# Kernel tuning notes

Hardware: AMD Instinct MI355X
Metric: run time of the kernel (lower is better)

The kernel has to match this reference:

```python
import jax, jax.numpy as jnp
import numpy as np

N = 131072          # total instances
G = 2048            # n_groups
MAX = 128           # padded max group size (>= true max by construction)
E = 256             # embed_dim
H = 8               # num_heads
D = E // H          # head dim


def setup_inputs() -> dict:
    key = jax.random.key(0)
    ks = jax.random.split(key, 9)
    # every group id appears at least once (matches torch.unique-derived groups)
    gids = jnp.concatenate([
        jnp.arange(G, dtype=jnp.int32),
        jax.random.randint(ks[0], (N - G,), 0, G, dtype=jnp.int32),
    ])
    return {
        "tree_preds": jax.random.normal(ks[1], (N, E), dtype=jnp.float32),
        "group_ids": gids,
        "query": jax.random.normal(ks[2], (1, 1, E), dtype=jnp.float32) * 0.02,
        "w_in": jax.random.normal(ks[3], (3 * E, E), dtype=jnp.float32) * 0.02,
        "b_in": jax.random.normal(ks[4], (3 * E,), dtype=jnp.float32) * 0.02,
        "w_out": jax.random.normal(ks[5], (E, E), dtype=jnp.float32) * 0.02,
        "b_out": jax.random.normal(ks[6], (E,), dtype=jnp.float32) * 0.02,
        "w_lin": jax.random.normal(ks[7], (1, E), dtype=jnp.float32) * 0.02,
        "b_lin": jax.random.normal(ks[8], (1,), dtype=jnp.float32) * 0.02,
    }


def _forward(tree_preds, group_ids, query, w_in, b_in, w_out, b_out, w_lin, b_lin):
    # --- scatter ragged groups into padded [G, MAX, E] tensor ---
    sorter = jnp.argsort(group_ids)                   # stable instance sorter
    sorted_gid = group_ids[sorter]
    sizes = jax.ops.segment_sum(jnp.ones_like(group_ids), group_ids,
                                num_segments=G)       # [G] group sizes
    offsets = jnp.cumsum(sizes) - sizes               # exclusive cumsum
    pos = jnp.arange(N, dtype=sizes.dtype) - offsets[sorted_gid]  # slot in group
    embs = jnp.zeros((G, MAX, E), dtype=tree_preds.dtype)
    embs = embs.at[sorted_gid, pos].set(tree_preds[sorter])
    kp_mask = jnp.arange(MAX)[None, :] >= sizes[:, None]          # [G, MAX] True=pad

    # --- single-query multi-head attention pooling ---
    wq, wk, wv = w_in[:E], w_in[E:2 * E], w_in[2 * E:]
    bq, bk, bv = b_in[:E], b_in[E:2 * E], b_in[2 * E:]
    q = (query.reshape(E) @ wq.T + bq).reshape(H, D)              # shared query
    k = (embs @ wk.T + bk).reshape(G, MAX, H, D)
    v = (embs @ wv.T + bv).reshape(G, MAX, H, D)
    scores = jnp.einsum("hd,gmhd->ghm", q, k) / jnp.sqrt(jnp.float32(D))
    scores = jnp.where(kp_mask[:, None, :], -jnp.inf, scores)
    attn = jax.nn.softmax(scores, axis=-1)                        # [G, H, MAX]
    pooled = jnp.einsum("ghm,gmhd->ghd", attn, v).reshape(G, E)
    pooled = pooled @ w_out.T + b_out                             # out_proj
    return pooled @ w_lin.T + b_lin                               # [G, 1]


def reference(tree_preds, group_ids, query, w_in, b_in, w_out, b_out, w_lin, b_lin):
    return _forward(tree_preds, group_ids, query, w_in, b_in,
                    w_out, b_out, w_lin, b_lin)
```

## Files before the change

### kernel.cpp

```cpp
#include <hip/hip_runtime.h>
#include <hip/hip_bf16.h>

#define EDIM 256
#define INV_SQRT_D 0.17677669529663688f
#define FXSCALE 1099511627776.0f

#define WS_QB   4096
#define WS_UB   4104
#define WS_C    4112
#define WS_QS   4128
#define WS_PU   4608
#define WB_BYTE_OFF 36864
#define ZM_BYTE_OFF 65536

typedef __attribute__((ext_vector_type(8))) short short8;
typedef __attribute__((ext_vector_type(4))) float f32x4;

__device__ __forceinline__ unsigned short f2bf(float f) {
  unsigned u = __float_as_uint(f);
  unsigned r = (u + 0x7fffu + ((u >> 16) & 1u)) >> 16;
  return (unsigned short)r;
}

__global__ __launch_bounds__(256) void zero_zm(unsigned long long* __restrict__ zm, int n) {
  const int i = blockIdx.x * 256 + threadIdx.x;
  const int stride = gridDim.x * 256;
  for (int k = i; k < n; k += stride) zm[k] = 0ull;
}

__global__ __launch_bounds__(256) void prep1(
    const float* __restrict__ query, const float* __restrict__ w_in,
    const float* __restrict__ b_in, const float* __restrict__ w_out,
    const float* __restrict__ w_lin, float* __restrict__ ws) {
  const int b = blockIdx.x, t = threadIdx.x;
  if (b < 32) {
    const int r = b * 8 + (t >> 5);
    const int l = t & 31;
    const float4 q0 = *(const float4*)(query + l * 8);
    const float4 q1 = *(const float4*)(query + l * 8 + 4);
    const float4 w0 = *(const float4*)(w_in + (size_t)r * EDIM + l * 8);
    const float4 w1 = *(const float4*)(w_in + (size_t)r * EDIM + l * 8 + 4);
    float a = q0.x * w0.x + q0.y * w0.y + q0.z * w0.z + q0.w * w0.w
            + q1.x * w1.x + q1.y * w1.y + q1.z * w1.z + q1.w * w1.w;
    for (int m = 16; m >= 1; m >>= 1) a += __shfl_xor(a, m, 32);
    if (l == 0) ws[WS_QS + r] = a + b_in[r];
  } else {
    const int k = b - 32;
    float acc = 0.f;
#pragma unroll
    for (int f = 0; f < 16; ++f) {
      const int fr = k * 16 + f;
      acc += w_lin[fr] * w_out[(size_t)fr * EDIM + t];
    }
    ws[WS_PU + k * EDIM + t] = acc;
  }
}

__global__ __launch_bounds__(256) void prep2(
    const float* __restrict__ w_in, const float* __restrict__ b_in,
    const float* __restrict__ b_out, const float* __restrict__ b_lin,
    const float* __restrict__ w_lin, float* __restrict__ ws,
    unsigned short* __restrict__ wb) {
  const int b = blockIdx.x, t = threadIdx.x;
  if (b < 8) {
    __shared__ float qh[32];
    if (t < 32) qh[t] = ws[WS_QS + b * 32 + t];
    __syncthreads();
    float a = 0.f;
#pragma unroll 8
    for (int d = 0; d < 32; ++d)
      a += qh[d] * w_in[(size_t)(EDIM + b * 32 + d) * EDIM + t];
    wb[b * EDIM + t] = f2bf(a * INV_SQRT_D);
  } else if (b < 16) {
    const int j = b - 8;
    __shared__ float uh[32];
    if (t < 32) {
      float s = 0.f;
#pragma unroll
      for (int k = 0; k < 16; ++k) s += ws[WS_PU + k * EDIM + j * 32 + t];
      uh[t] = s;
    }
    __syncthreads();
    float a = 0.f;
#pragma unroll 8
    for (int d = 0; d < 32; ++d)
      a += uh[d] * w_in[(size_t)(2 * EDIM + j * 32 + d) * EDIM + t];
    wb[(8 + j) * EDIM + t] = f2bf(a);
  } else {
    __shared__ float us[EDIM];
    float s = 0.f;
#pragma unroll
    for (int k = 0; k < 16; ++k) s += ws[WS_PU + k * EDIM + t];
    us[t] = s;
    __syncthreads();
    if (t < 8) {
      float qb = 0.f, ub = 0.f;
#pragma unroll 4
      for (int d = 0; d < 32; ++d) {
        qb += ws[WS_QS + t * 32 + d] * b_in[EDIM + t * 32 + d];
        ub += us[t * 32 + d] * b_in[2 * EDIM + t * 32 + d];
      }
      ws[WS_QB + t] = qb * INV_SQRT_D;
      ws[WS_UB + t] = ub;
    }
    if (t == 0) {
      float c = b_lin[0];
      for (int f = 0; f < EDIM; ++f) c += w_lin[f] * b_out[f];
      ws[WS_C] = c;
    }
  }
}

#define LROW 260
__global__ __launch_bounds__(256, 4) void main_mfma(
    const float* __restrict__ x, const int* __restrict__ gid,
    const float* __restrict__ ws, const unsigned short* __restrict__ wb,
    unsigned long long* __restrict__ zm, int n_items) {
  __shared__ unsigned short lds[4 * 16 * LROW];
  const int t = threadIdx.x;
  const int lane = t & 63, wave = t >> 6;
  unsigned short* my = lds + wave * 16 * LROW;
  const int wid = (int)(blockIdx.x * 4 + wave);
  const int nw = (int)(gridDim.x * 4);
  const int n = lane & 15, quad = lane >> 4;
  const int h = n & 7, isw = (n >> 3) & 1;

  short8 bfrag[8];
#pragma unroll
  for (int kc = 0; kc < 8; ++kc)
    bfrag[kc] = *(const short8*)(wb + n * EDIM + quad * 8 + kc * 32);

  const float qb = ws[WS_QB + h];
  const float ub = ws[WS_UB + h];

  const int ntiles = (n_items + 15) >> 4;
  for (int tile = wid; tile < ntiles; tile += nw) {
    const int base = tile << 4;
    const bool full = (base + 16 <= n_items);
    int4 g4;
    if (full) {
      g4 = *(const int4*)(gid + base + quad * 4);
#pragma unroll
      for (int i = 0; i < 16; ++i) {
        const float4 v = *(const float4*)(x + (size_t)(base + i) * EDIM + lane * 4);
        union { unsigned short s[4]; unsigned long long ll; } pk;
        pk.s[0] = f2bf(v.x); pk.s[1] = f2bf(v.y);
        pk.s[2] = f2bf(v.z); pk.s[3] = f2bf(v.w);
        *(unsigned long long*)(my + i * LROW + lane * 4) = pk.ll;
      }
    } else {
      int gg[4];
      for (int r = 0; r < 4; ++r) {
        const int m = quad * 4 + r;
        gg[r] = (base + m < n_items) ? gid[base + m] : 0;
      }
      g4.x = gg[0]; g4.y = gg[1]; g4.z = gg[2]; g4.w = gg[3];
      for (int i = 0; i < 16; ++i) {
        union { unsigned short s[4]; unsigned long long ll; } pk;
        if (base + i < n_items) {
          const float4 v = *(const float4*)(x + (size_t)(base + i) * EDIM + lane * 4);
          pk.s[0] = f2bf(v.x); pk.s[1] = f2bf(v.y);
          pk.s[2] = f2bf(v.z); pk.s[3] = f2bf(v.w);
        } else pk.ll = 0ull;
        *(unsigned long long*)(my + i * LROW + lane * 4) = pk.ll;
      }
    }
    f32x4 acc = {0.f, 0.f, 0.f, 0.f};
#pragma unroll
    for (int kc = 0; kc < 8; ++kc) {
      const short8 a = *(const short8*)(my + n * LROW + quad * 8 + kc * 32);
      acc = __builtin_amdgcn_mfma_f32_16x16x32_bf16(a, bfrag[kc], acc, 0, 0, 0);
    }
#pragma unroll
    for (int r = 0; r < 4; ++r) {
      const int m = quad * 4 + r;
      const float mine = acc[r];
      const float partner = __shfl_xor(mine, 8, 64);
      const float sv = (isw ? partner : mine) + qb;
      const float wv = (isw ? mine : partner) + ub;
      const float e = __expf(sv);
      const float val = isw ? e * wv : e;
      const int g = (r == 0) ? g4.x : (r == 1) ? g4.y : (r == 2) ? g4.z : g4.w;
      if (base + m < n_items) {
        const long long qv = llrintf(val * FXSCALE);
        atomicAdd(zm + ((size_t)g * 16 + h * 2 + isw), (unsigned long long)qv);
      }
    }
  }
}

__global__ __launch_bounds__(256) void finalize(
    const long long* __restrict__ zm, const float* __restrict__ ws,
    float* __restrict__ out, int G) {
  const int g = blockIdx.x * blockDim.x + threadIdx.x;
  if (g >= G) return;
  double acc = (double)ws[WS_C];
  const long long* row = zm + (size_t)g * 16;
#pragma unroll
  for (int hh = 0; hh < 8; ++hh)
    acc += (double)row[hh * 2 + 1] / (double)row[hh * 2];
  out[g] = (float)acc;
}

__device__ __forceinline__ float dot16_reduce(const float4 (&W)[16],
                                              const float4 xv, const int lane) {
  float p[16];
#pragma unroll
  for (int j = 0; j < 16; ++j)
    p[j] = W[j].x * xv.x + W[j].y * xv.y + W[j].z * xv.z + W[j].w * xv.w;
#pragma unroll
  for (int j = 0; j < 8; ++j) {
    float send = (lane & 1) ? p[j] : p[j + 8];
    float keep = (lane & 1) ? p[j + 8] : p[j];
    p[j] = keep + __shfl_xor(send, 1, 64);
  }
#pragma unroll
  for (int j = 0; j < 4; ++j) {
    float send = (lane & 2) ? p[j] : p[j + 4];
    float keep = (lane & 2) ? p[j + 4] : p[j];
    p[j] = keep + __shfl_xor(send, 2, 64);
  }
#pragma unroll
  for (int j = 0; j < 2; ++j) {
    float send = (lane & 4) ? p[j] : p[j + 2];
    float keep = (lane & 4) ? p[j + 2] : p[j];
    p[j] = keep + __shfl_xor(send, 4, 64);
  }
  {
    float send = (lane & 8) ? p[0] : p[1];
    float keep = (lane & 8) ? p[1] : p[0];
    p[0] = keep + __shfl_xor(send, 8, 64);
  }
  p[0] += __shfl_xor(p[0], 16, 64);
  p[0] += __shfl_xor(p[0], 32, 64);
  return p[0];
}

__device__ __forceinline__ int bitrev4(const int l4) {
  return ((l4 & 1) << 3) | ((l4 & 2) << 1) | ((l4 & 4) >> 1) | ((l4 & 8) >> 3);
}

__global__ __launch_bounds__(256) void group_scan(
    const float* __restrict__ x, const int* __restrict__ gid,
    const float* __restrict__ query, const float* __restrict__ w_in,
    const float* __restrict__ b_in, const float* __restrict__ w_out,
    const float* __restrict__ b_out, const float* __restrict__ w_lin,
    const float* __restrict__ b_lin, float* __restrict__ out, int n_items) {
  const int g = blockIdx.x;
  const int t = threadIdx.x;
  __shared__ float Wl[16 * EDIM];
  __shared__ float querys[EDIM], wls[EDIM], qs[EDIM], us[EDIM];
  __shared__ float qbias[8], ubias[8], csh;
  __shared__ float part[4][16], sums[16];

  querys[t] = query[t];
  wls[t] = w_lin[t];
  __syncthreads();
  {
    float acc = 0.f;
    const float4* wr = (const float4*)(w_in + (size_t)t * EDIM);
    for (int f4 = 0; f4 < EDIM / 4; ++f4) {
      float4 wv = wr[f4];
      int f = f4 * 4;
      acc += wv.x * querys[f] + wv.y * querys[f + 1] + wv.z * querys[f + 2] + wv.w * querys[f + 3];
    }
    qs[t] = acc + b_in[t];
  }
  {
    float acc = 0.f;
    for (int f = 0; f < EDIM; ++f) acc += wls[f] * w_out[(size_t)f * EDIM + t];
    us[t] = acc;
  }
  __syncthreads();
  for (int j = 0; j < 8; ++j) {
    float a = 0.f;
    for (int d = 0; d < 32; ++d)
      a += qs[j * 32 + d] * w_in[(size_t)(EDIM + j * 32 + d) * EDIM + t];
    Wl[j * EDIM + t] = a * INV_SQRT_D;
  }
  for (int j = 0; j < 8; ++j) {
    float a = 0.f;
    for (int d = 0; d < 32; ++d)
      a += us[j * 32 + d] * w_in[(size_t)(2 * EDIM + j * 32 + d) * EDIM + t];
    Wl[(8 + j) * EDIM + t] = a;
  }
  if (t < 8) {
    float qb = 0.f, ub = 0.f;
    for (int d = 0; d < 32; ++d) {
      qb += qs[t * 32 + d] * b_in[EDIM + t * 32 + d];
      ub += us[t * 32 + d] * b_in[2 * EDIM + t * 32 + d];
    }
    qbias[t] = qb * INV_SQRT_D;
    ubias[t] = ub;
  }
  if (t == 0) {
    float c = b_lin[0];
    for (int f = 0; f < EDIM; ++f) c += wls[f] * b_out[f];
    csh = c;
  }
  __syncthreads();

  const int lane = t & 63;
  const int wave = t >> 6;
  float4 W[16];
#pragma unroll
  for (int j = 0; j < 16; ++j)
    W[j] = *(const float4*)(Wl + j * EDIM + lane * 4);
  const int jv = bitrev4(lane & 15);
  const int h = jv & 7;
  const int isw = (jv >> 3) & 1;
  const float bias_s = qbias[h];
  const float bias_w = ubias[h];

  float accv = 0.f;
  const int nchunk = (n_items + 63) >> 6;
  for (int c = wave; c < nchunk; c += 4) {
    const int i0 = c << 6;
    const int ii = i0 + lane;
    const int gi = (ii < n_items) ? gid[ii] : -1;
    unsigned long long mk = __ballot(gi == g);
    while (mk) {
      const int bpos = __ffsll(mk) - 1;
      mk &= mk - 1;
      const int i = i0 + bpos;
      const float4 xv = *(const float4*)(x + (size_t)i * EDIM + lane * 4);
      const float p0 = dot16_reduce(W, xv, lane);
      const float tpair = __shfl_xor(p0, 1, 64);
      const float sv = (isw ? tpair : p0) + bias_s;
      const float wv = (isw ? p0 : tpair) + bias_w;
      const float e = __expf(sv);
      accv += isw ? e * wv : e;
    }
  }
  if (lane < 16) part[wave][h * 2 + isw] = accv;
  __syncthreads();
  if (t < 16) sums[t] = part[0][t] + part[1][t] + part[2][t] + part[3][t];
  __syncthreads();
  if (t == 0) {
    double acc = (double)csh;
    for (int hh = 0; hh < 8; ++hh)
      acc += (double)sums[2 * hh + 1] / (double)sums[2 * hh];
    out[g] = (float)acc;
  }
}

extern "C" void kernel_launch(void* const* d_in, const int* in_sizes, int n_in,
                              void* d_out, int out_size, void* d_ws, size_t ws_size,
                              hipStream_t stream) {
  const float* tree_preds = (const float*)d_in[0];
  const int* group_ids = (const int*)d_in[1];
  const float* query = (const float*)d_in[2];
  const float* w_in = (const float*)d_in[3];
  const float* b_in = (const float*)d_in[4];
  const float* w_out = (const float*)d_in[5];
  const float* b_out = (const float*)d_in[6];
  const float* w_lin = (const float*)d_in[7];
  const float* b_lin = (const float*)d_in[8];
  float* out = (float*)d_out;

  const int N = in_sizes[1];
  const int G = out_size;

  const size_t needA = (size_t)ZM_BYTE_OFF + (size_t)G * 16 * 8;
  if (ws_size >= needA) {
    float* ws = (float*)d_ws;
    unsigned short* wb = (unsigned short*)((char*)d_ws + WB_BYTE_OFF);
    unsigned long long* zm = (unsigned long long*)((char*)d_ws + ZM_BYTE_OFF);
    zero_zm<<<64, 256, 0, stream>>>(zm, G * 16);
    prep1<<<48, 256, 0, stream>>>(query, w_in, b_in, w_out, w_lin, ws);
    prep2<<<17, 256, 0, stream>>>(w_in, b_in, b_out, b_lin, w_lin, ws, wb);
    main_mfma<<<1024, 256, 0, stream>>>(tree_preds, group_ids, ws, wb, zm, N);
    finalize<<<(G + 255) / 256, 256, 0, stream>>>((const long long*)zm, ws, out, G);
  } else {
    group_scan<<<G, 256, 0, stream>>>(tree_preds, group_ids, query, w_in, b_in,
                                      w_out, b_out, w_lin, b_lin, out, N);
  }
}
```

Baseline: 221.2 us.

## Load MFMA A-fragments directly from global, drop LDS staging, fold zeroing into prep1

The main kernel now has each lane load the fp32 row slice it needs for the MFMA A operand directly from global memory. It converts that slice to bf16 with packed conversions and feeds the MFMA without staging the tile through LDS. This removes the LDS writes and reads and frees LDS, which may allow higher occupancy. The cost is strided 32-byte per-lane global accesses instead of fully coalesced row loads. The separate zeroing kernel is merged into extra blocks of prep1 to save one kernel launch.

```diff
diff --git a/kernel.cpp b/kernel.cpp
--- a/kernel.cpp
+++ b/kernel.cpp
@@ -22,16 +22,18 @@
   return (unsigned short)r;
 }
 
-__global__ __launch_bounds__(256) void zero_zm(unsigned long long* __restrict__ zm, int n) {
-  const int i = blockIdx.x * 256 + threadIdx.x;
-  const int stride = gridDim.x * 256;
-  for (int k = i; k < n; k += stride) zm[k] = 0ull;
+__device__ __forceinline__ unsigned int cvt_pk_bf16(float a, float b) {
+  __hip_bfloat162 t = __float22bfloat162_rn(float2{a, b});
+  unsigned int u;
+  __builtin_memcpy(&u, &t, 4);
+  return u;
 }
 
 __global__ __launch_bounds__(256) void prep1(
     const float* __restrict__ query, const float* __restrict__ w_in,
     const float* __restrict__ b_in, const float* __restrict__ w_out,
-    const float* __restrict__ w_lin, float* __restrict__ ws) {
+    const float* __restrict__ w_lin, float* __restrict__ ws,
+    unsigned long long* __restrict__ zm, int nzm) {
   const int b = blockIdx.x, t = threadIdx.x;
   if (b < 32) {
     const int r = b * 8 + (t >> 5);
@@ -44,7 +46,7 @@
             + q1.x * w1.x + q1.y * w1.y + q1.z * w1.z + q1.w * w1.w;
     for (int m = 16; m >= 1; m >>= 1) a += __shfl_xor(a, m, 32);
     if (l == 0) ws[WS_QS + r] = a + b_in[r];
-  } else {
+  } else if (b < 48) {
     const int k = b - 32;
     float acc = 0.f;
 #pragma unroll
@@ -53,6 +55,8 @@
       acc += w_lin[fr] * w_out[(size_t)fr * EDIM + t];
     }
     ws[WS_PU + k * EDIM + t] = acc;
+  } else {
+    for (int k = (b - 48) * 256 + t; k < nzm; k += 16 * 256) zm[k] = 0ull;
   }
 }
 
@@ -111,17 +115,12 @@
   }
 }
 
-#define LROW 260
 __global__ __launch_bounds__(256, 4) void main_mfma(
     const float* __restrict__ x, const int* __restrict__ gid,
     const float* __restrict__ ws, const unsigned short* __restrict__ wb,
     unsigned long long* __restrict__ zm, int n_items) {
-  __shared__ unsigned short lds[4 * 16 * LROW];
   const int t = threadIdx.x;
-  const int lane = t & 63, wave = t >> 6;
-  unsigned short* my = lds + wave * 16 * LROW;
-  const int wid = (int)(blockIdx.x * 4 + wave);
-  const int nw = (int)(gridDim.x * 4);
+  const int lane = t & 63;
   const int n = lane & 15, quad = lane >> 4;
   const int h = n & 7, isw = (n >> 3) & 1;
 
@@ -133,47 +132,52 @@
   const float qb = ws[WS_QB + h];
   const float ub = ws[WS_UB + h];
 
+  const int wid = (int)(blockIdx.x * (blockDim.x >> 6) + (t >> 6));
+  const int nw = (int)(gridDim.x * (blockDim.x >> 6));
   const int ntiles = (n_items + 15) >> 4;
+
   for (int tile = wid; tile < ntiles; tile += nw) {
     const int base = tile << 4;
-    const bool full = (base + 16 <= n_items);
+    const float* rowp = x + (size_t)(base + n) * EDIM + quad * 8;
+    f32x4 acc = {0.f, 0.f, 0.f, 0.f};
     int4 g4;
-    if (full) {
+    if (base + 16 <= n_items) {
       g4 = *(const int4*)(gid + base + quad * 4);
 #pragma unroll
-      for (int i = 0; i < 16; ++i) {
-        const float4 v = *(const float4*)(x + (size_t)(base + i) * EDIM + lane * 4);
-        union { unsigned short s[4]; unsigned long long ll; } pk;
-        pk.s[0] = f2bf(v.x); pk.s[1] = f2bf(v.y);
-        pk.s[2] = f2bf(v.z); pk.s[3] = f2bf(v.w);
-        *(unsigned long long*)(my + i * LROW + lane * 4) = pk.ll;
+      for (int kc = 0; kc < 8; ++kc) {
+        const float4 v0 = *(const float4*)(rowp + kc * 32);
+        const float4 v1 = *(const float4*)(rowp + kc * 32 + 4);
+        union { short8 s; unsigned int u[4]; } a;
+        a.u[0] = cvt_pk_bf16(v0.x, v0.y);
+        a.u[1] = cvt_pk_bf16(v0.z, v0.w);
+        a.u[2] = cvt_pk_bf16(v1.x, v1.y);
+        a.u[3] = cvt_pk_bf16(v1.z, v1.w);
+        acc = __builtin_amdgcn_mfma_f32_16x16x32_bf16(a.s, bfrag[kc], acc, 0, 0, 0);
       }
     } else {
       int gg[4];
-      for (int r = 0; r < 4; ++r) {
-        const int m = quad * 4 + r;
-        gg[r] = (base + m < n_items) ? gid[base + m] : 0;
+#pragma unroll
+      for (int r = 0; r < 4; ++r)
+        gg[r] = (base + quad * 4 + r < n_items) ? gid[base + quad * 4 + r] : 0;
+      g4.x = gg[0]; g4.y = gg[1]; g4.z = gg[2]; g4.w = gg[3];
+      const bool live = (base + n < n_items);
+#pragma unroll
+      for (int kc = 0; kc < 8; ++kc) {
+        float4 v0 = {0.f, 0.f, 0.f, 0.f}, v1 = {0.f, 0.f, 0.f, 0.f};
+        if (live) {
+          v0 = *(const float4*)(rowp + kc * 32);
+          v1 = *(const float4*)(rowp + kc * 32 + 4);
+        }
+        union { short8 s; unsigned int u[4]; } a;
+        a.u[0] = cvt_pk_bf16(v0.x, v0.y);
+        a.u[1] = cvt_pk_bf16(v0.z, v0.w);
+        a.u[2] = cvt_pk_bf16(v1.x, v1.y);
+        a.u[3] = cvt_pk_bf16(v1.z, v1.w);
+        acc = __builtin_amdgcn_mfma_f32_16x16x32_bf16(a.s, bfrag[kc], acc, 0, 0, 0);
       }
-      g4.x = gg[0]; g4.y = gg[1]; g4.z = gg[2]; g4.w = gg[3];
-      for (int i = 0; i < 16; ++i) {
-        union { unsigned short s[4]; unsigned long long ll; } pk;
-        if (base + i < n_items) {
-          const float4 v = *(const float4*)(x + (size_t)(base + i) * EDIM + lane * 4);
-          pk.s[0] = f2bf(v.x); pk.s[1] = f2bf(v.y);
-          pk.s[2] = f2bf(v.z); pk.s[3] = f2bf(v.w);
-        } else pk.ll = 0ull;
-        *(unsigned long long*)(my + i * LROW + lane * 4) = pk.ll;
-      }
-    }
-    f32x4 acc = {0.f, 0.f, 0.f, 0.f};
-#pragma unroll
-    for (int kc = 0; kc < 8; ++kc) {
-      const short8 a = *(const short8*)(my + n * LROW + quad * 8 + kc * 32);
-      acc = __builtin_amdgcn_mfma_f32_16x16x32_bf16(a, bfrag[kc], acc, 0, 0, 0);
     }
 #pragma unroll
     for (int r = 0; r < 4; ++r) {
-      const int m = quad * 4 + r;
       const float mine = acc[r];
       const float partner = __shfl_xor(mine, 8, 64);
       const float sv = (isw ? partner : mine) + qb;
@@ -181,7 +185,7 @@
       const float e = __expf(sv);
       const float val = isw ? e * wv : e;
       const int g = (r == 0) ? g4.x : (r == 1) ? g4.y : (r == 2) ? g4.z : g4.w;
-      if (base + m < n_items) {
+      if (base + quad * 4 + r < n_items) {
         const long long qv = llrintf(val * FXSCALE);
         atomicAdd(zm + ((size_t)g * 16 + h * 2 + isw), (unsigned long long)qv);
       }
@@ -366,8 +370,7 @@
     float* ws = (float*)d_ws;
     unsigned short* wb = (unsigned short*)((char*)d_ws + WB_BYTE_OFF);
     unsigned long long* zm = (unsigned long long*)((char*)d_ws + ZM_BYTE_OFF);
-    zero_zm<<<64, 256, 0, stream>>>(zm, G * 16);
-    prep1<<<48, 256, 0, stream>>>(query, w_in, b_in, w_out, w_lin, ws);
+    prep1<<<64, 256, 0, stream>>>(query, w_in, b_in, w_out, w_lin, ws, zm, G * 16);
     prep2<<<17, 256, 0, stream>>>(w_in, b_in, b_out, b_lin, w_lin, ws, wb);
     main_mfma<<<1024, 256, 0, stream>>>(tree_preds, group_ids, ws, wb, zm, N);
     finalize<<<(G + 255) / 256, 256, 0, stream>>>((const long long*)zm, ws, out, G);
```

New measurement: 219.4 us. No clear change (-0.8%).
